# Kernel tuning notes

Hardware: AMD Instinct MI355X
Metric: run time of the kernel (lower is better)

The kernel has to match this reference:

```python
import jax, jax.numpy as jnp
import numpy as np

MAX_DEPTH = 7
DEPTH_SIZES = [4 ** d for d in range(1, MAX_DEPTH + 1)]  # nodes per depth
N_NODES = sum(DEPTH_SIZES)  # 21844
N_TIMES = 48
HIDDEN = 1024
ENC_DIM = 256
B, S = 128, 32


def setup_inputs() -> dict:
    key = jax.random.key(0)
    k = jax.random.split(key, 6)
    return {
        "prefix_embedding": jax.random.normal(k[0], (B, S, HIDDEN), dtype=jnp.float32),
        "emb_matrix": jax.random.normal(k[1], (N_NODES, ENC_DIM), dtype=jnp.float32) * 0.02,
        "W_key": jax.random.normal(k[2], (HIDDEN, ENC_DIM), dtype=jnp.float32) * (1.0 / np.sqrt(ENC_DIM)),
        "b_key": jax.random.normal(k[3], (HIDDEN,), dtype=jnp.float32) * 0.01,
        "W_time": jax.random.normal(k[4], (N_TIMES, HIDDEN), dtype=jnp.float32) * (1.0 / np.sqrt(HIDDEN)),
        "b_time": jax.random.normal(k[5], (N_TIMES,), dtype=jnp.float32) * 0.01,
    }


def reference(prefix_embedding, emb_matrix, W_key, b_key, W_time, b_time):
    # keys = embedding_to_key(make_embedding_matrix(...)): [N_NODES, HIDDEN]
    keys = emb_matrix @ W_key.T + b_key
    # bmm(prefix [B,S,H], keys^T): keys identical across batch -> shared einsum
    scores = jnp.einsum("bsh,nh->bsn", prefix_embedding, keys)  # [B,S,N_NODES]
    # multitask: per-depth gather of the contiguous node block + log_softmax
    locations = []
    off = 0
    for n in DEPTH_SIZES:
        locations.append(jax.nn.log_softmax(scores[..., off:off + n], axis=-1))
        off += n
    time = jax.nn.log_softmax(prefix_embedding @ W_time.T + b_time, axis=-1)  # [B,S,N_TIMES]
    return tuple(locations) + (time,)
```

## Files before the change

### kernel.cpp

```cpp
#include <hip/hip_runtime.h>

#define NNODES 21844
#define ENC 256
#define HID 1024
#define ROWS 4096
#define NTIMES 48

typedef __attribute__((ext_vector_type(8))) short bf16x8;
typedef __attribute__((ext_vector_type(8))) unsigned short u16x8;
typedef __attribute__((ext_vector_type(4))) float f32x4;

__device__ const int g_off[8] = {0, 4, 20, 84, 340, 1364, 5460, 21844};

__device__ inline unsigned short f2bf(float f) {
  unsigned int u = __float_as_uint(f);
  u += 0x7FFF + ((u >> 16) & 1);
  return (unsigned short)(u >> 16);
}

__device__ inline int depth_of(int c) {
  return (c >= 4) + (c >= 20) + (c >= 84) + (c >= 340) + (c >= 1364) + (c >= 5460);
}

__global__ __launch_bounds__(256) void prep(const float* __restrict__ prefix,
                                            const float* __restrict__ emb,
                                            const float* __restrict__ Wk,
                                            const float* __restrict__ Wt,
                                            unsigned short* __restrict__ Pb16,
                                            unsigned short* __restrict__ Eb,
                                            unsigned short* __restrict__ WkT,
                                            float* __restrict__ WtT,
                                            float* __restrict__ S) {
  int bid = blockIdx.x, tid = threadIdx.x;
  if (bid < 4096) {
    int i = bid * 256 + tid;
    float4 v = reinterpret_cast<const float4*>(prefix)[i];
    ushort4 o; o.x = f2bf(v.x); o.y = f2bf(v.y); o.z = f2bf(v.z); o.w = f2bf(v.w);
    reinterpret_cast<ushort4*>(Pb16)[i] = o;
  } else if (bid < 9557) {
    int i = (bid - 4096) * 256 + tid;
    float4 v = reinterpret_cast<const float4*>(emb)[i];
    ushort4 o; o.x = f2bf(v.x); o.y = f2bf(v.y); o.z = f2bf(v.z); o.w = f2bf(v.w);
    reinterpret_cast<ushort4*>(Eb)[i] = o;
  } else if (bid < 10581) {
    int i = (bid - 9557) * 256 + tid;
    int e = i >> 10, h = i & 1023;
    WkT[i] = f2bf(Wk[h * ENC + e]);
  } else if (bid < 10773) {
    int i = (bid - 10581) * 256 + tid;
    int k = i / NTIMES, c = i % NTIMES;
    WtT[i] = Wt[c * HID + k];
  } else {
    int i = (bid - 10773) * 256 + tid;
    reinterpret_cast<float4*>(S)[i] = float4{0.f, 0.f, 0.f, 0.f};
  }
}

__global__ __launch_bounds__(256) void p2_mfma(const unsigned short* __restrict__ Ab,
                                               const unsigned short* __restrict__ Bb,
                                               unsigned short* __restrict__ P2) {
  int lane = threadIdx.x & 63, w = threadIdx.x >> 6;
  int lr = lane & 15, lg = lane >> 4;
  int m0 = blockIdx.y * 64 + w * 16;
  int nb = blockIdx.x * 64;
  f32x4 acc[4];
#pragma unroll
  for (int n = 0; n < 4; ++n) acc[n] = f32x4{0.f, 0.f, 0.f, 0.f};
  const unsigned short* Ap = Ab + (long)(m0 + lr) * HID + lg * 8;
  for (int kk = 0; kk < 32; ++kk) {
    bf16x8 a = *reinterpret_cast<const bf16x8*>(Ap + kk * 32);
#pragma unroll
    for (int n = 0; n < 4; ++n) {
      bf16x8 b = *reinterpret_cast<const bf16x8*>(Bb + (long)(nb + n * 16 + lr) * HID + kk * 32 + lg * 8);
      acc[n] = __builtin_amdgcn_mfma_f32_16x16x32_bf16(a, b, acc[n], 0, 0, 0);
    }
  }
#pragma unroll
  for (int n = 0; n < 4; ++n)
#pragma unroll
    for (int j = 0; j < 4; ++j)
      P2[(m0 + lg * 4 + j) * ENC + nb + n * 16 + lr] = f2bf(acc[n][j]);
}

template <int BF16S>
__global__ __launch_bounds__(256) void gemm_stash(const unsigned short* __restrict__ P2,
                                                  const unsigned short* __restrict__ E,
                                                  unsigned short* __restrict__ stash,
                                                  float* __restrict__ outp,
                                                  float* __restrict__ S) {
  __shared__ unsigned short SH[2][2][128 * 64];
  int tid = threadIdx.x;
  int lane = tid & 63, w = tid >> 6;
  int lr = lane & 15, lg = lane >> 4;
  int wr = w >> 1, wc = w & 1;
  int m0 = blockIdx.x * 128, n0 = blockIdx.y * 128;
  int rr = tid >> 3, c8 = tid & 7;

  f32x4 acc[4][4];
#pragma unroll
  for (int m = 0; m < 4; ++m)
#pragma unroll
    for (int n = 0; n < 4; ++n) acc[m][n] = f32x4{0.f, 0.f, 0.f, 0.f};

#define STAGE(buf, kt)                                                                    \
  _Pragma("unroll") for (int r = 0; r < 4; ++r) {                                         \
    const unsigned short* ga = P2 + (long)(m0 + r * 32 + rr) * ENC + (kt) * 64 + c8 * 8;  \
    __builtin_amdgcn_global_load_lds(                                                     \
        (const __attribute__((address_space(1))) unsigned int*)ga,                        \
        (__attribute__((address_space(3))) unsigned int*)(&SH[buf][0][r * 2048 + w * 512]), \
        16, 0, 0);                                                                        \
    int er = n0 + r * 32 + rr;                                                            \
    if (er > NNODES - 1) er = NNODES - 1;                                                 \
    const unsigned short* gb = E + (long)er * ENC + (kt) * 64 + c8 * 8;                   \
    __builtin_amdgcn_global_load_lds(                                                     \
        (const __attribute__((address_space(1))) unsigned int*)gb,                        \
        (__attribute__((address_space(3))) unsigned int*)(&SH[buf][1][r * 2048 + w * 512]), \
        16, 0, 0);                                                                        \
  }

  STAGE(0, 0)
  __syncthreads();
  for (int kt = 0; kt < 4; ++kt) {
    int cur = kt & 1;
    if (kt < 3) { STAGE(cur ^ 1, kt + 1) }
    const unsigned short* As = &SH[cur][0][0];
    const unsigned short* Bs = &SH[cur][1][0];
#pragma unroll
    for (int kk = 0; kk < 2; ++kk) {
      bf16x8 a[4], b[4];
#pragma unroll
      for (int m = 0; m < 4; ++m)
        a[m] = *reinterpret_cast<const bf16x8*>(As + (wr * 64 + m * 16 + lr) * 64 + kk * 32 + lg * 8);
#pragma unroll
      for (int n = 0; n < 4; ++n)
        b[n] = *reinterpret_cast<const bf16x8*>(Bs + (wc * 64 + n * 16 + lr) * 64 + kk * 32 + lg * 8);
#pragma unroll
      for (int m = 0; m < 4; ++m)
#pragma unroll
        for (int n = 0; n < 4; ++n)
          acc[m][n] = __builtin_amdgcn_mfma_f32_16x16x32_bf16(a[m], b[n], acc[m][n], 0, 0, 0);
    }
    __syncthreads();
  }
#undef STAGE

  int rbase = m0 + wr * 64 + lg * 4;
  int hstart = n0 + wc * 64;
#pragma unroll
  for (int n = 0; n < 4; ++n) {
    int gc = hstart + n * 16 + lr;
    if (gc < NNODES) {
      int d = depth_of(gc);
      long ob = ((long)g_off[d] << 12) + (gc - g_off[d]);
      int sh = 2 * (d + 1);
#pragma unroll
      for (int m = 0; m < 4; ++m)
#pragma unroll
        for (int j = 0; j < 4; ++j) {
          int row = rbase + m * 16 + j;
          long idx = ob + ((long)row << sh);
          if (BF16S) stash[idx] = f2bf(acc[m][n][j]);
          else       outp[idx]  = acc[m][n][j];
        }
    }
  }
  int dlo = depth_of(hstart);
  int hend = hstart + 63; if (hend > NNODES - 1) hend = NNODES - 1;
  int dhi = depth_of(hend);
  int cd[4];
#pragma unroll
  for (int n = 0; n < 4; ++n) {
    int gc = hstart + n * 16 + lr;
    cd[n] = (gc < NNODES) ? depth_of(gc) : 99;
  }
#pragma unroll
  for (int m = 0; m < 4; ++m)
#pragma unroll
    for (int n = 0; n < 4; ++n)
#pragma unroll
      for (int j = 0; j < 4; ++j) acc[m][n][j] = __expf(acc[m][n][j]);
  for (int dt = dlo; dt <= dhi; ++dt) {
#pragma unroll
    for (int m = 0; m < 4; ++m) {
      float s[4] = {0.f, 0.f, 0.f, 0.f};
#pragma unroll
      for (int n = 0; n < 4; ++n) {
        bool use = (cd[n] == dt);
#pragma unroll
        for (int j = 0; j < 4; ++j) s[j] += use ? acc[m][n][j] : 0.f;
      }
#pragma unroll
      for (int j = 0; j < 4; ++j)
#pragma unroll
        for (int o = 1; o < 16; o <<= 1) s[j] += __shfl_xor(s[j], o);
      if (lr == 0) {
#pragma unroll
        for (int j = 0; j < 4; ++j)
          atomicAdd(&S[dt * ROWS + rbase + m * 16 + j], s[j]);
      }
    }
  }
}

template <int BF16S>
__global__ __launch_bounds__(256) void sub_write(const unsigned short* __restrict__ stash,
                                                 const float* __restrict__ S,
                                                 float* __restrict__ out) {
  int tid = threadIdx.x;
  long blk = blockIdx.x;
  long base[4];
  u16x8 u[4];
  float4 f0[4], f1[4];
#pragma unroll
  for (int i = 0; i < 4; ++i) base[i] = blk * 8192 + i * 2048 + tid * 8;
  if (BF16S) {
#pragma unroll
    for (int i = 0; i < 4; ++i) u[i] = *reinterpret_cast<const u16x8*>(stash + base[i]);
  } else {
#pragma unroll
    for (int i = 0; i < 4; ++i) {
      f0[i] = reinterpret_cast<const float4*>(out + base[i])[0];
      f1[i] = reinterpret_cast<const float4*>(out + base[i])[1];
    }
  }
#pragma unroll
  for (int i = 0; i < 4; ++i) {
    int cc = (int)blk * 4 + i;
    int d = (cc >= 8) + (cc >= 40) + (cc >= 168) + (cc >= 680) + (cc >= 2728) + (cc >= 10920);
    long bd = (d == 0) ? 0L : (d == 1) ? 16384L : (d == 2) ? 81920L : (d == 3) ? 344064L
            : (d == 4) ? 1392640L : (d == 5) ? 5586944L : 22364160L;
    long rel = base[i] - bd;
    const float* sp = S + d * ROWS;
    float v[8];
    if (BF16S) {
#pragma unroll
      for (int j = 0; j < 8; ++j) v[j] = __uint_as_float((unsigned)(unsigned short)u[i][j] << 16);
    } else {
      v[0] = f0[i].x; v[1] = f0[i].y; v[2] = f0[i].z; v[3] = f0[i].w;
      v[4] = f1[i].x; v[5] = f1[i].y; v[6] = f1[i].z; v[7] = f1[i].w;
    }
    float4 o0, o1;
    if (d == 0) {
      int r0 = (int)(rel >> 2);
      float l0 = __logf(sp[r0]), l1 = __logf(sp[r0 + 1]);
      o0 = float4{v[0] - l0, v[1] - l0, v[2] - l0, v[3] - l0};
      o1 = float4{v[4] - l1, v[5] - l1, v[6] - l1, v[7] - l1};
    } else {
      int row = (int)(rel >> (2 * (d + 1)));
      float l = __logf(sp[row]);
      o0 = float4{v[0] - l, v[1] - l, v[2] - l, v[3] - l};
      o1 = float4{v[4] - l, v[5] - l, v[6] - l, v[7] - l};
    }
    reinterpret_cast<float4*>(out + base[i])[0] = o0;
    reinterpret_cast<float4*>(out + base[i])[1] = o1;
  }
}

__global__ __launch_bounds__(256) void time_head(const float* __restrict__ prefix,
                                                 const float* __restrict__ WtT,
                                                 const float* __restrict__ bt,
                                                 float* __restrict__ out) {
  int lane = threadIdx.x & 63;
  int row = blockIdx.x * 4 + (threadIdx.x >> 6);
  const float4* pr = reinterpret_cast<const float4*>(prefix + (long)row * HID);
  float acc = -3.4e38f;
  if (lane < NTIMES) {
    float a0 = 0.f, a1 = 0.f, a2 = 0.f, a3 = 0.f;
    for (int q = 0; q < HID / 4; ++q) {
      float4 pv = pr[q];
      const float* wrow = WtT + q * 4 * NTIMES;
      a0 += pv.x * wrow[lane];
      a1 += pv.y * wrow[NTIMES + lane];
      a2 += pv.z * wrow[2 * NTIMES + lane];
      a3 += pv.w * wrow[3 * NTIMES + lane];
    }
    acc = (a0 + a1) + (a2 + a3) + bt[lane];
  }
  float m = acc;
#pragma unroll
  for (int d = 32; d; d >>= 1) m = fmaxf(m, __shfl_xor(m, d));
  float e = (lane < NTIMES) ? __expf(acc - m) : 0.f;
  float s = e;
#pragma unroll
  for (int d = 32; d; d >>= 1) s += __shfl_xor(s, d);
  if (lane < NTIMES) out[89473024 + row * NTIMES + lane] = acc - m - __logf(s);
}

extern "C" void kernel_launch(void* const* d_in, const int* in_sizes, int n_in,
                              void* d_out, int out_size, void* d_ws, size_t ws_size,
                              hipStream_t stream) {
  const float* prefix = (const float*)d_in[0];
  const float* emb    = (const float*)d_in[1];
  const float* Wk     = (const float*)d_in[2];
  const float* Wt     = (const float*)d_in[4];
  const float* bt     = (const float*)d_in[5];
  float* out = (float*)d_out;
  char* ws = (char*)d_ws;

  unsigned short* P2    = (unsigned short*)(ws + 0);
  unsigned short* Eb    = (unsigned short*)(ws + 2097152);
  unsigned short* WkT   = (unsigned short*)(ws + 13281280);
  unsigned short* Pb16  = (unsigned short*)(ws + 13805568);
  float*          WtT   = (float*)(ws + 22194176);
  float*          S     = (float*)(ws + 22390784);
  unsigned short* stash = (unsigned short*)(ws + 22505472);
  const size_t WS_NEED_STASH = 22505472UL + 178946048UL;

  bool big = ws_size >= WS_NEED_STASH;

  prep<<<10801, 256, 0, stream>>>(prefix, emb, Wk, Wt, Pb16, Eb, WkT, WtT, S);

  p2_mfma<<<dim3(4, 64), 256, 0, stream>>>(Pb16, WkT, P2);

  if (big) {
    gemm_stash<1><<<dim3(32, 171), 256, 0, stream>>>(P2, Eb, stash, out, S);
    sub_write<1><<<10922, 256, 0, stream>>>(stash, S, out);
  } else {
    gemm_stash<0><<<dim3(32, 171), 256, 0, stream>>>(P2, Eb, stash, out, S);
    sub_write<0><<<10922, 256, 0, stream>>>(stash, S, out);
  }

  time_head<<<1024, 256, 0, stream>>>(prefix, WtT, bt, out);
}
```

Before: 348.0 us.

## Widen score GEMM tile to 128x256, precompute log-sum, coarsen sub_write

Measured after the change: 371.1 us. +6.6%, slower.

```diff
diff --git a/kernel.cpp b/kernel.cpp
--- a/kernel.cpp
+++ b/kernel.cpp
@@ -83,17 +83,18 @@
 }
 
 template <int BF16S>
-__global__ __launch_bounds__(256) void gemm_stash(const unsigned short* __restrict__ P2,
+__global__ __launch_bounds__(512) void gemm_stash(const unsigned short* __restrict__ P2,
                                                   const unsigned short* __restrict__ E,
                                                   unsigned short* __restrict__ stash,
                                                   float* __restrict__ outp,
                                                   float* __restrict__ S) {
-  __shared__ unsigned short SH[2][2][128 * 64];
+  __shared__ unsigned short Abuf[2][128 * 64];
+  __shared__ unsigned short Bbuf[2][256 * 64];
   int tid = threadIdx.x;
   int lane = tid & 63, w = tid >> 6;
   int lr = lane & 15, lg = lane >> 4;
-  int wr = w >> 1, wc = w & 1;
-  int m0 = blockIdx.x * 128, n0 = blockIdx.y * 128;
+  int wr = w >> 2, wc = w & 3;
+  int m0 = blockIdx.x * 128, n0 = blockIdx.y * 256;
   int rr = tid >> 3, c8 = tid & 7;
 
   f32x4 acc[4][4];
@@ -102,20 +103,22 @@
 #pragma unroll
     for (int n = 0; n < 4; ++n) acc[m][n] = f32x4{0.f, 0.f, 0.f, 0.f};
 
-#define STAGE(buf, kt)                                                                    \
-  _Pragma("unroll") for (int r = 0; r < 4; ++r) {                                         \
-    const unsigned short* ga = P2 + (long)(m0 + r * 32 + rr) * ENC + (kt) * 64 + c8 * 8;  \
-    __builtin_amdgcn_global_load_lds(                                                     \
-        (const __attribute__((address_space(1))) unsigned int*)ga,                        \
-        (__attribute__((address_space(3))) unsigned int*)(&SH[buf][0][r * 2048 + w * 512]), \
-        16, 0, 0);                                                                        \
-    int er = n0 + r * 32 + rr;                                                            \
-    if (er > NNODES - 1) er = NNODES - 1;                                                 \
-    const unsigned short* gb = E + (long)er * ENC + (kt) * 64 + c8 * 8;                   \
-    __builtin_amdgcn_global_load_lds(                                                     \
-        (const __attribute__((address_space(1))) unsigned int*)gb,                        \
-        (__attribute__((address_space(3))) unsigned int*)(&SH[buf][1][r * 2048 + w * 512]), \
-        16, 0, 0);                                                                        \
+#define STAGE(buf, kt)                                                                     \
+  _Pragma("unroll") for (int r = 0; r < 2; ++r) {                                          \
+    const unsigned short* ga = P2 + (long)(m0 + r * 64 + rr) * ENC + (kt) * 64 + c8 * 8;   \
+    __builtin_amdgcn_global_load_lds(                                                      \
+        (const __attribute__((address_space(1))) unsigned int*)ga,                         \
+        (__attribute__((address_space(3))) unsigned int*)(&Abuf[buf][r * 4096 + tid * 8]), \
+        16, 0, 0);                                                                         \
+  }                                                                                        \
+  _Pragma("unroll") for (int r = 0; r < 4; ++r) {                                          \
+    int er = n0 + r * 64 + rr;                                                             \
+    if (er > NNODES - 1) er = NNODES - 1;                                                  \
+    const unsigned short* gb = E + (long)er * ENC + (kt) * 64 + c8 * 8;                    \
+    __builtin_amdgcn_global_load_lds(                                                      \
+        (const __attribute__((address_space(1))) unsigned int*)gb,                         \
+        (__attribute__((address_space(3))) unsigned int*)(&Bbuf[buf][r * 4096 + tid * 8]), \
+        16, 0, 0);                                                                         \
   }
 
   STAGE(0, 0)
@@ -123,8 +126,8 @@
   for (int kt = 0; kt < 4; ++kt) {
     int cur = kt & 1;
     if (kt < 3) { STAGE(cur ^ 1, kt + 1) }
-    const unsigned short* As = &SH[cur][0][0];
-    const unsigned short* Bs = &SH[cur][1][0];
+    const unsigned short* As = &Abuf[cur][0];
+    const unsigned short* Bs = &Bbuf[cur][0];
 #pragma unroll
     for (int kk = 0; kk < 2; ++kk) {
       bf16x8 a[4], b[4];
@@ -202,35 +205,41 @@
   }
 }
 
+__global__ __launch_bounds__(256) void lse_log(const float* __restrict__ S,
+                                               float* __restrict__ L) {
+  int i = blockIdx.x * 256 + threadIdx.x;
+  L[i] = __logf(S[i]);
+}
+
 template <int BF16S>
 __global__ __launch_bounds__(256) void sub_write(const unsigned short* __restrict__ stash,
-                                                 const float* __restrict__ S,
+                                                 const float* __restrict__ Lse,
                                                  float* __restrict__ out) {
   int tid = threadIdx.x;
   long blk = blockIdx.x;
-  long base[4];
-  u16x8 u[4];
-  float4 f0[4], f1[4];
-#pragma unroll
-  for (int i = 0; i < 4; ++i) base[i] = blk * 8192 + i * 2048 + tid * 8;
+  long base[8];
+  u16x8 u[8];
+  float4 f0[8], f1[8];
+#pragma unroll
+  for (int i = 0; i < 8; ++i) base[i] = blk * 16384 + i * 2048 + tid * 8;
   if (BF16S) {
 #pragma unroll
-    for (int i = 0; i < 4; ++i) u[i] = *reinterpret_cast<const u16x8*>(stash + base[i]);
+    for (int i = 0; i < 8; ++i) u[i] = *reinterpret_cast<const u16x8*>(stash + base[i]);
   } else {
 #pragma unroll
-    for (int i = 0; i < 4; ++i) {
+    for (int i = 0; i < 8; ++i) {
       f0[i] = reinterpret_cast<const float4*>(out + base[i])[0];
       f1[i] = reinterpret_cast<const float4*>(out + base[i])[1];
     }
   }
 #pragma unroll
-  for (int i = 0; i < 4; ++i) {
-    int cc = (int)blk * 4 + i;
+  for (int i = 0; i < 8; ++i) {
+    int cc = (int)blk * 8 + i;
     int d = (cc >= 8) + (cc >= 40) + (cc >= 168) + (cc >= 680) + (cc >= 2728) + (cc >= 10920);
     long bd = (d == 0) ? 0L : (d == 1) ? 16384L : (d == 2) ? 81920L : (d == 3) ? 344064L
             : (d == 4) ? 1392640L : (d == 5) ? 5586944L : 22364160L;
     long rel = base[i] - bd;
-    const float* sp = S + d * ROWS;
+    const float* lp = Lse + d * ROWS;
     float v[8];
     if (BF16S) {
 #pragma unroll
@@ -242,12 +251,12 @@
     float4 o0, o1;
     if (d == 0) {
       int r0 = (int)(rel >> 2);
-      float l0 = __logf(sp[r0]), l1 = __logf(sp[r0 + 1]);
+      float l0 = lp[r0], l1 = lp[r0 + 1];
       o0 = float4{v[0] - l0, v[1] - l0, v[2] - l0, v[3] - l0};
       o1 = float4{v[4] - l1, v[5] - l1, v[6] - l1, v[7] - l1};
     } else {
       int row = (int)(rel >> (2 * (d + 1)));
-      float l = __logf(sp[row]);
+      float l = lp[row];
       o0 = float4{v[0] - l, v[1] - l, v[2] - l, v[3] - l};
       o1 = float4{v[4] - l, v[5] - l, v[6] - l, v[7] - l};
     }
@@ -303,8 +312,9 @@
   unsigned short* Pb16  = (unsigned short*)(ws + 13805568);
   float*          WtT   = (float*)(ws + 22194176);
   float*          S     = (float*)(ws + 22390784);
-  unsigned short* stash = (unsigned short*)(ws + 22505472);
-  const size_t WS_NEED_STASH = 22505472UL + 178946048UL;
+  float*          Lse   = (float*)(ws + 22505472);
+  unsigned short* stash = (unsigned short*)(ws + 22620160);
+  const size_t WS_NEED_STASH = 22620160UL + 178946048UL;
 
   bool big = ws_size >= WS_NEED_STASH;
 
@@ -313,11 +323,13 @@
   p2_mfma<<<dim3(4, 64), 256, 0, stream>>>(Pb16, WkT, P2);
 
   if (big) {
-    gemm_stash<1><<<dim3(32, 171), 256, 0, stream>>>(P2, Eb, stash, out, S);
-    sub_write<1><<<10922, 256, 0, stream>>>(stash, S, out);
+    gemm_stash<1><<<dim3(32, 86), 512, 0, stream>>>(P2, Eb, stash, out, S);
+    lse_log<<<112, 256, 0, stream>>>(S, Lse);
+    sub_write<1><<<5461, 256, 0, stream>>>(stash, Lse, out);
   } else {
-    gemm_stash<0><<<dim3(32, 171), 256, 0, stream>>>(P2, Eb, stash, out, S);
-    sub_write<0><<<10922, 256, 0, stream>>>(stash, S, out);
+    gemm_stash<0><<<dim3(32, 86), 512, 0, stream>>>(P2, Eb, stash, out, S);
+    lse_log<<<112, 256, 0, stream>>>(S, Lse);
+    sub_write<0><<<5461, 256, 0, stream>>>(stash, Lse, out);
   }
 
   time_head<<<1024, 256, 0, stream>>>(prefix, WtT, bt, out);
```
